# Kernel tuning notes

Measured on AMD Instinct MI355X. Metric: run time of the kernel, lower is better.

Reference implementation:

```python
import jax, jax.numpy as jnp
import numpy as np

N = 500_000   # active voxels
K = 27        # 3x3x3 kernel offsets
CIN = 32
COUT = 64
EPS = 1e-5


def setup_inputs() -> dict:
    key = jax.random.key(0)
    ks = jax.random.split(key, 9)
    x_feats = jax.random.normal(ks[0], (N, CIN), jnp.float32)
    # neighbor map: for each kernel offset k and output voxel i, index of the
    # input voxel contributing through offset k (submanifold conv, stride=1)
    nbr = jax.random.randint(ks[1], (K, N), 0, N, jnp.int32)
    s1 = 1.0 / np.sqrt(K * CIN)
    s2 = 1.0 / np.sqrt(K * COUT)
    w1 = jax.random.normal(ks[2], (K, CIN, COUT), jnp.float32) * s1
    w2 = jax.random.normal(ks[3], (K, COUT, COUT), jnp.float32) * s2
    g1 = jnp.ones((COUT,), jnp.float32)
    b1 = jnp.zeros((COUT,), jnp.float32)
    g2 = jnp.ones((COUT,), jnp.float32)
    b2 = jnp.zeros((COUT,), jnp.float32)
    wid = jax.random.normal(ks[4], (CIN, COUT), jnp.float32) * (1.0 / np.sqrt(CIN))
    gid = jnp.ones((COUT,), jnp.float32)
    bid = jnp.zeros((COUT,), jnp.float32)
    return {"x_feats": x_feats, "nbr": nbr, "w1": w1, "g1": g1, "b1": b1,
            "w2": w2, "g2": g2, "b2": b2, "wid": wid, "gid": gid, "bid": bid}


def _sparse_conv(feats, nbr, W):
    # feats [N, Cin], nbr [K, N], W [K, Cin, Cout]
    # scan over the fixed 27 kernel offsets: gather -> matmul -> accumulate
    def step(acc, kw):
        idx, w = kw
        return acc + feats[idx] @ w, None
    out0 = jnp.zeros((feats.shape[0], W.shape[-1]), feats.dtype)
    out, _ = jax.lax.scan(step, out0, (nbr, W))
    return out


def _bn(x, g, b):
    # training-mode BatchNorm1d over the voxel axis (biased variance, as torch)
    m = jnp.mean(x, axis=0)
    v = jnp.var(x, axis=0)
    return (x - m) * jax.lax.rsqrt(v + EPS) * g + b


def reference(x_feats, nbr, w1, g1, b1, w2, g2, b2, wid, gid, bid):
    h = jax.nn.relu(_bn(_sparse_conv(x_feats, nbr, w1), g1, b1))
    h = _bn(_sparse_conv(h, nbr, w2), g2, b2)
    ident = _bn(x_feats @ wid, gid, bid)
    return jax.nn.relu(h + ident)
```

## Files before the change

### kernel.cpp

```cpp
#include <hip/hip_runtime.h>

#define NV 500000
#define KOFF 27
#define CIN_ 32
#define COUT_ 64
#define EPS_ 1e-5f

typedef __attribute__((ext_vector_type(8))) _Float16 half8;
typedef __attribute__((ext_vector_type(4))) float floatx4;


__global__ void zero_stats_kernel(float* __restrict__ s) {
  if (threadIdx.x < 384) s[threadIdx.x] = 0.f;
}

__global__ __launch_bounds__(256) void cast_x_kernel(
    const float* __restrict__ x, _Float16* __restrict__ xh) {
  size_t q = (size_t)blockIdx.x * 256 + threadIdx.x;
  if (q >= (size_t)NV * CIN_ / 8) return;
  const float4* xp = (const float4*)x;
  float4 a = xp[2 * q], b = xp[2 * q + 1];
  half8 h;
  h[0] = (_Float16)a.x; h[1] = (_Float16)a.y; h[2] = (_Float16)a.z; h[3] = (_Float16)a.w;
  h[4] = (_Float16)b.x; h[5] = (_Float16)b.y; h[6] = (_Float16)b.z; h[7] = (_Float16)b.w;
  ((half8*)xh)[q] = h;
}

__global__ void wtrans_kernel(const float* __restrict__ w,
                              _Float16* __restrict__ wT, int CI) {
  int t = blockIdx.x * 256 + threadIdx.x;
  int total = KOFF * CI * COUT_;
  if (t >= total) return;
  int k = t / (CI * COUT_);
  int r = t % (CI * COUT_);
  int co = r / CI;
  int ci = r % CI;
  wT[t] = (_Float16)w[(k * CI + ci) * COUT_ + co];
}


template<int CI>
__device__ __forceinline__ void stageB(const _Float16* __restrict__ wT,
                                       _Float16* __restrict__ lds,
                                       int k0, int kp, int tid) {
  __syncthreads();
  const int segs = CI / 8;
  const int chunks = kp * COUT_ * segs;
  for (int idx = tid; idx < chunks; idx += 1024) {
    int row = idx / segs;
    int s = idx - row * segs;
    half8 v = *(const half8*)(wT + ((size_t)k0 * COUT_ + row) * CI + s * 8);
    *(half8*)(lds + (size_t)row * (CI + 8) + s * 8) = v;
  }
  __syncthreads();
}

template<int CI, int KPC, int D>
__device__ __forceinline__ void run_phase(
    const half8* __restrict__ fp, const int* __restrict__ nbr,
    const _Float16* __restrict__ lds, int k0,
    int v0, int v1, int m, int quad, floatx4 acc[2][4]) {
  constexpr int SEG = CI / 32;
  constexpr int ROWH8 = CI / 8;

  int j0[KPC], j1[KPC];
#pragma unroll
  for (int k = 0; k < KPC; ++k) {
    j0[k] = nbr[(k0 + k) * NV + v0] * ROWH8;
    j1[k] = nbr[(k0 + k) * NV + v1] * ROWH8;
  }

  half8 ring[D][2][SEG];
#pragma unroll
  for (int p = 0; p < D; ++p) {
#pragma unroll
    for (int s = 0; s < SEG; ++s) {
      ring[p][0][s] = fp[(size_t)j0[p] + s * 4 + quad];
      ring[p][1][s] = fp[(size_t)j1[p] + s * 4 + quad];
    }
  }

#pragma unroll
  for (int k = 0; k < KPC; ++k) {
    const _Float16* bk = lds + (size_t)k * COUT_ * (CI + 8);
#pragma unroll
    for (int s = 0; s < SEG; ++s) {
#pragma unroll
      for (int nf = 0; nf < 4; ++nf) {
        half8 bf = *(const half8*)(bk + (nf * 16 + m) * (CI + 8) + s * 32 + quad * 8);
        acc[0][nf] = __builtin_amdgcn_mfma_f32_16x16x32_f16(ring[k % D][0][s], bf, acc[0][nf], 0, 0, 0);
        acc[1][nf] = __builtin_amdgcn_mfma_f32_16x16x32_f16(ring[k % D][1][s], bf, acc[1][nf], 0, 0, 0);
      }
    }
    if (k + D < KPC) {
#pragma unroll
      for (int s = 0; s < SEG; ++s) {
        ring[k % D][0][s] = fp[(size_t)j0[k + D] + s * 4 + quad];
        ring[k % D][1][s] = fp[(size_t)j1[k + D] + s * 4 + quad];
      }
    }
  }
}

template<int CI, bool WF16>
__global__ __launch_bounds__(1024, 4) void conv_mfma_v3(
    const _Float16* __restrict__ feats, const int* __restrict__ nbr,
    const _Float16* __restrict__ wT, float* __restrict__ outF,
    _Float16* __restrict__ outH) {
  constexpr int LDSH = (CI == 64) ? 7 * 64 * 72 : 9 * 64 * 40;
  __shared__ __align__(16) _Float16 ldsB[LDSH];

  int tid = threadIdx.x;
  int wave = tid >> 6, lane = tid & 63;
  int m = lane & 15, quad = lane >> 4;
  int vbase = (blockIdx.x * 16 + wave) * 32;
  int v0 = vbase + m;
  int v1 = vbase + 16 + m;
  v0 = v0 < NV ? v0 : NV - 1;
  v1 = v1 < NV ? v1 : NV - 1;
  const half8* fp = (const half8*)feats;

  floatx4 acc[2][4];
#pragma unroll
  for (int g = 0; g < 2; ++g)
#pragma unroll
    for (int nf = 0; nf < 4; ++nf) acc[g][nf] = (floatx4){0.f, 0.f, 0.f, 0.f};

  if constexpr (CI == 64) {
    stageB<CI>(wT, ldsB, 0, 7, tid);
    run_phase<CI, 7, 3>(fp, nbr, ldsB, 0, v0, v1, m, quad, acc);
    stageB<CI>(wT, ldsB, 7, 7, tid);
    run_phase<CI, 7, 3>(fp, nbr, ldsB, 7, v0, v1, m, quad, acc);
    stageB<CI>(wT, ldsB, 14, 7, tid);
    run_phase<CI, 7, 3>(fp, nbr, ldsB, 14, v0, v1, m, quad, acc);
    stageB<CI>(wT, ldsB, 21, 6, tid);
    run_phase<CI, 6, 3>(fp, nbr, ldsB, 21, v0, v1, m, quad, acc);
  } else {
    stageB<CI>(wT, ldsB, 0, 9, tid);
    run_phase<CI, 9, 4>(fp, nbr, ldsB, 0, v0, v1, m, quad, acc);
    stageB<CI>(wT, ldsB, 9, 9, tid);
    run_phase<CI, 9, 4>(fp, nbr, ldsB, 9, v0, v1, m, quad, acc);
    stageB<CI>(wT, ldsB, 18, 9, tid);
    run_phase<CI, 9, 4>(fp, nbr, ldsB, 18, v0, v1, m, quad, acc);
  }

#pragma unroll
  for (int g = 0; g < 2; ++g)
#pragma unroll
    for (int nf = 0; nf < 4; ++nf)
#pragma unroll
      for (int r = 0; r < 4; ++r) {
        int row = vbase + g * 16 + quad * 4 + r;
        if (row < NV) {
          size_t o = (size_t)row * COUT_ + nf * 16 + m;
          if (WF16) outH[o] = (_Float16)acc[g][nf][r];
          else outF[o] = acc[g][nf][r];
        }
      }
}


__global__ __launch_bounds__(256) void stats_f16_kernel(
    const _Float16* __restrict__ y, float* __restrict__ sums) {
  int lane = threadIdx.x & 63;
  int r0 = blockIdx.x * 4 + (threadIdx.x >> 6);
  int stride = gridDim.x * 4;
  float s = 0.f, ss = 0.f;
  for (int r = r0; r < NV; r += stride) {
    float v = (float)y[(size_t)r * COUT_ + lane];
    s += v;
    ss = fmaf(v, v, ss);
  }
  __shared__ float ls[128];
  if (threadIdx.x < 128) ls[threadIdx.x] = 0.f;
  __syncthreads();
  atomicAdd(&ls[lane], s);
  atomicAdd(&ls[64 + lane], ss);
  __syncthreads();
  if (threadIdx.x < 128) atomicAdd(&sums[threadIdx.x], ls[threadIdx.x]);
}

__global__ __launch_bounds__(256) void stats_f32_kernel(
    const float* __restrict__ y, float* __restrict__ sums) {
  int lane = threadIdx.x & 63;
  int r0 = blockIdx.x * 4 + (threadIdx.x >> 6);
  int stride = gridDim.x * 4;
  float s = 0.f, ss = 0.f;
  for (int r = r0; r < NV; r += stride) {
    float v = y[(size_t)r * COUT_ + lane];
    s += v;
    ss = fmaf(v, v, ss);
  }
  __shared__ float ls[128];
  if (threadIdx.x < 128) ls[threadIdx.x] = 0.f;
  __syncthreads();
  atomicAdd(&ls[lane], s);
  atomicAdd(&ls[64 + lane], ss);
  __syncthreads();
  if (threadIdx.x < 128) atomicAdd(&sums[threadIdx.x], ls[threadIdx.x]);
}

__global__ __launch_bounds__(256) void ident_stats_kernel(
    const float* __restrict__ x, const float* __restrict__ wid,
    float* __restrict__ sums) {
  int lane = threadIdx.x & 63;
  int wv = blockIdx.x * 4 + (threadIdx.x >> 6);
  int nw = gridDim.x * 4;
  float wcol[CIN_];
#pragma unroll
  for (int ci = 0; ci < CIN_; ++ci) wcol[ci] = wid[ci * COUT_ + lane];
  float s = 0.f, ss = 0.f;
  for (int v = wv; v < NV; v += nw) {
    const float* xr = x + (size_t)v * CIN_;
    float d = 0.f;
#pragma unroll
    for (int ci = 0; ci < CIN_; ++ci) d = fmaf(xr[ci], wcol[ci], d);
    s += d;
    ss = fmaf(d, d, ss);
  }
  __shared__ float ls[128];
  if (threadIdx.x < 128) ls[threadIdx.x] = 0.f;
  __syncthreads();
  atomicAdd(&ls[lane], s);
  atomicAdd(&ls[64 + lane], ss);
  __syncthreads();
  if (threadIdx.x < 128) atomicAdd(&sums[threadIdx.x], ls[threadIdx.x]);
}

__global__ void finalize_kernel(const float* __restrict__ sums,
                                const float* __restrict__ g,
                                const float* __restrict__ b,
                                float* __restrict__ out) {
  int c = threadIdx.x;
  float m = sums[c] * (1.0f / NV);
  float var = sums[64 + c] * (1.0f / NV) - m * m;
  float sc = g[c] / sqrtf(var + EPS_);
  out[c] = sc;
  out[64 + c] = b[c] - m * sc;
}

__global__ __launch_bounds__(256) void bnrelu_f16_kernel(
    _Float16* __restrict__ y, const float* __restrict__ scsh) {
  size_t q = (size_t)blockIdx.x * 256 + threadIdx.x;
  if (q >= (size_t)NV * COUT_ / 8) return;
  int c0 = (int)(q & 7) * 8;
  half8 v = ((const half8*)y)[q];
#pragma unroll
  for (int jj = 0; jj < 8; ++jj) {
    float f = fmaxf(fmaf((float)v[jj], scsh[c0 + jj], scsh[64 + c0 + jj]), 0.f);
    v[jj] = (_Float16)f;
  }
  ((half8*)y)[q] = v;
}

__global__ __launch_bounds__(256) void final_kernel(
    const float* __restrict__ x, const float* __restrict__ wid,
    float* __restrict__ y2out, const float* __restrict__ ss2,
    const float* __restrict__ ssid) {
  int lane = threadIdx.x & 63;
  int wv = blockIdx.x * 4 + (threadIdx.x >> 6);
  int nw = gridDim.x * 4;
  float wcol[CIN_];
#pragma unroll
  for (int ci = 0; ci < CIN_; ++ci) wcol[ci] = wid[ci * COUT_ + lane];
  float sc2 = ss2[lane], sh2 = ss2[64 + lane];
  float sci = ssid[lane], shi = ssid[64 + lane];
  for (int v = wv; v < NV; v += nw) {
    const float* xr = x + (size_t)v * CIN_;
    float d = 0.f;
#pragma unroll
    for (int ci = 0; ci < CIN_; ++ci) d = fmaf(xr[ci], wcol[ci], d);
    size_t o = (size_t)v * COUT_ + lane;
    float r = fmaf(y2out[o], sc2, sh2) + fmaf(d, sci, shi);
    y2out[o] = fmaxf(r, 0.f);
  }
}

extern "C" void kernel_launch(void* const* d_in, const int* in_sizes, int n_in,
                              void* d_out, int out_size, void* d_ws, size_t ws_size,
                              hipStream_t stream) {
  const float* x   = (const float*)d_in[0];
  const int*   nbr = (const int*)d_in[1];
  const float* w1  = (const float*)d_in[2];
  const float* g1  = (const float*)d_in[3];
  const float* b1  = (const float*)d_in[4];
  const float* w2  = (const float*)d_in[5];
  const float* g2  = (const float*)d_in[6];
  const float* b2  = (const float*)d_in[7];
  const float* wid = (const float*)d_in[8];
  const float* gid = (const float*)d_in[9];
  const float* bid = (const float*)d_in[10];
  float* out = (float*)d_out;

  _Float16* y1h = (_Float16*)d_ws;
  _Float16* xh  = y1h + (size_t)NV * COUT_;
  _Float16* wT1 = xh + (size_t)NV * CIN_;
  _Float16* wT2 = wT1 + KOFF * COUT_ * CIN_;
  float*    st  = (float*)(wT2 + KOFF * COUT_ * COUT_);

  const int NWG = (NV + 511) / 512;

  zero_stats_kernel<<<1, 384, 0, stream>>>(st);
  cast_x_kernel<<<(NV * CIN_ / 8 + 255) / 256, 256, 0, stream>>>(x, xh);
  wtrans_kernel<<<(KOFF * CIN_ * COUT_ + 255) / 256, 256, 0, stream>>>(w1, wT1, CIN_);
  wtrans_kernel<<<(KOFF * COUT_ * COUT_ + 255) / 256, 256, 0, stream>>>(w2, wT2, COUT_);

  conv_mfma_v3<CIN_, true><<<NWG, 1024, 0, stream>>>(xh, nbr, wT1, nullptr, y1h);
  stats_f16_kernel<<<2048, 256, 0, stream>>>(y1h, st + 0);
  ident_stats_kernel<<<2048, 256, 0, stream>>>(x, wid, st + 256);
  finalize_kernel<<<1, 64, 0, stream>>>(st + 0, g1, b1, st + 384);
  finalize_kernel<<<1, 64, 0, stream>>>(st + 256, gid, bid, st + 640);
  bnrelu_f16_kernel<<<(NV * COUT_ / 8 + 255) / 256, 256, 0, stream>>>(y1h, st + 384);

  conv_mfma_v3<COUT_, false><<<NWG, 1024, 0, stream>>>(y1h, nbr, wT2, out, nullptr);
  stats_f32_kernel<<<2048, 256, 0, stream>>>(out, st + 128);
  finalize_kernel<<<1, 64, 0, stream>>>(st + 128, g2, b2, st + 512);
  final_kernel<<<4096, 256, 0, stream>>>(x, wid, out, st + 512, st + 640);
}
```

Measured before the change: 1.187 ms.

## Fuse BN statistics into conv epilogues and merge prep kernels

```diff
diff --git a/kernel.cpp b/kernel.cpp
--- a/kernel.cpp
+++ b/kernel.cpp
@@ -14,28 +14,67 @@
   if (threadIdx.x < 384) s[threadIdx.x] = 0.f;
 }
 
-__global__ __launch_bounds__(256) void cast_x_kernel(
-    const float* __restrict__ x, _Float16* __restrict__ xh) {
-  size_t q = (size_t)blockIdx.x * 256 + threadIdx.x;
-  if (q >= (size_t)NV * CIN_ / 8) return;
-  const float4* xp = (const float4*)x;
-  float4 a = xp[2 * q], b = xp[2 * q + 1];
-  half8 h;
-  h[0] = (_Float16)a.x; h[1] = (_Float16)a.y; h[2] = (_Float16)a.z; h[3] = (_Float16)a.w;
-  h[4] = (_Float16)b.x; h[5] = (_Float16)b.y; h[6] = (_Float16)b.z; h[7] = (_Float16)b.w;
-  ((half8*)xh)[q] = h;
-}
-
-__global__ void wtrans_kernel(const float* __restrict__ w,
-                              _Float16* __restrict__ wT, int CI) {
-  int t = blockIdx.x * 256 + threadIdx.x;
-  int total = KOFF * CI * COUT_;
-  if (t >= total) return;
-  int k = t / (CI * COUT_);
-  int r = t % (CI * COUT_);
-  int co = r / CI;
-  int ci = r % CI;
-  wT[t] = (_Float16)w[(k * CI + ci) * COUT_ + co];
+#define CAST_BLKS ((NV * CIN_ / 8 + 255) / 256)
+#define WT1_BLKS ((KOFF * CIN_ * COUT_ + 255) / 256)
+#define WT2_BLKS ((KOFF * COUT_ * COUT_ + 255) / 256)
+#define IDST_BLKS 2048
+
+__global__ __launch_bounds__(256) void prep_kernel(
+    const float* __restrict__ x, _Float16* __restrict__ xh,
+    const float* __restrict__ w1, _Float16* __restrict__ wT1,
+    const float* __restrict__ w2, _Float16* __restrict__ wT2,
+    const float* __restrict__ wid, float* __restrict__ idsums) {
+  int b = blockIdx.x;
+  if (b < CAST_BLKS) {
+    size_t q = (size_t)b * 256 + threadIdx.x;
+    if (q >= (size_t)NV * CIN_ / 8) return;
+    const float4* xp = (const float4*)x;
+    float4 a = xp[2 * q], c = xp[2 * q + 1];
+    half8 h;
+    h[0] = (_Float16)a.x; h[1] = (_Float16)a.y; h[2] = (_Float16)a.z; h[3] = (_Float16)a.w;
+    h[4] = (_Float16)c.x; h[5] = (_Float16)c.y; h[6] = (_Float16)c.z; h[7] = (_Float16)c.w;
+    ((half8*)xh)[q] = h;
+  } else if (b < CAST_BLKS + WT1_BLKS) {
+    int t = (b - CAST_BLKS) * 256 + threadIdx.x;
+    if (t >= KOFF * CIN_ * COUT_) return;
+    int k = t / (CIN_ * COUT_);
+    int r = t % (CIN_ * COUT_);
+    int co = r / CIN_;
+    int ci = r % CIN_;
+    wT1[t] = (_Float16)w1[(k * CIN_ + ci) * COUT_ + co];
+  } else if (b < CAST_BLKS + WT1_BLKS + WT2_BLKS) {
+    int t = (b - CAST_BLKS - WT1_BLKS) * 256 + threadIdx.x;
+    if (t >= KOFF * COUT_ * COUT_) return;
+    int k = t / (COUT_ * COUT_);
+    int r = t % (COUT_ * COUT_);
+    int co = r / COUT_;
+    int ci = r % COUT_;
+    wT2[t] = (_Float16)w2[(k * COUT_ + ci) * COUT_ + co];
+  } else {
+    int bb = b - CAST_BLKS - WT1_BLKS - WT2_BLKS;
+    int lane = threadIdx.x & 63;
+    int wv = bb * 4 + (threadIdx.x >> 6);
+    int nw = IDST_BLKS * 4;
+    float wcol[CIN_];
+#pragma unroll
+    for (int ci = 0; ci < CIN_; ++ci) wcol[ci] = wid[ci * COUT_ + lane];
+    float s = 0.f, ss = 0.f;
+    for (int v = wv; v < NV; v += nw) {
+      const float* xr = x + (size_t)v * CIN_;
+      float d = 0.f;
+#pragma unroll
+      for (int ci = 0; ci < CIN_; ++ci) d = fmaf(xr[ci], wcol[ci], d);
+      s += d;
+      ss = fmaf(d, d, ss);
+    }
+    __shared__ float ls[128];
+    if (threadIdx.x < 128) ls[threadIdx.x] = 0.f;
+    __syncthreads();
+    atomicAdd(&ls[lane], s);
+    atomicAdd(&ls[64 + lane], ss);
+    __syncthreads();
+    if (threadIdx.x < 128) atomicAdd(&idsums[threadIdx.x], ls[threadIdx.x]);
+  }
 }
 
 
@@ -103,12 +142,13 @@
 }
 
 template<int CI, bool WF16>
-__global__ __launch_bounds__(1024, 4) void conv_mfma_v3(
+__global__ __launch_bounds__(1024, 4) void conv_mfma_v9(
     const _Float16* __restrict__ feats, const int* __restrict__ nbr,
     const _Float16* __restrict__ wT, float* __restrict__ outF,
-    _Float16* __restrict__ outH) {
+    _Float16* __restrict__ outH, float* __restrict__ stOut) {
   constexpr int LDSH = (CI == 64) ? 7 * 64 * 72 : 9 * 64 * 40;
   __shared__ __align__(16) _Float16 ldsB[LDSH];
+  __shared__ float bs[128];
 
   int tid = threadIdx.x;
   int wave = tid >> 6, lane = tid & 63;
@@ -119,6 +159,8 @@
   v0 = v0 < NV ? v0 : NV - 1;
   v1 = v1 < NV ? v1 : NV - 1;
   const half8* fp = (const half8*)feats;
+
+  if (tid < 128) bs[tid] = 0.f;
 
   floatx4 acc[2][4];
 #pragma unroll
@@ -144,6 +186,9 @@
     run_phase<CI, 9, 4>(fp, nbr, ldsB, 18, v0, v1, m, quad, acc);
   }
 
+  float s4[4], q4[4];
+#pragma unroll
+  for (int nf = 0; nf < 4; ++nf) { s4[nf] = 0.f; q4[nf] = 0.f; }
 #pragma unroll
   for (int g = 0; g < 2; ++g)
 #pragma unroll
@@ -152,119 +197,77 @@
       for (int r = 0; r < 4; ++r) {
         int row = vbase + g * 16 + quad * 4 + r;
         if (row < NV) {
+          float v = acc[g][nf][r];
           size_t o = (size_t)row * COUT_ + nf * 16 + m;
-          if (WF16) outH[o] = (_Float16)acc[g][nf][r];
-          else outF[o] = acc[g][nf][r];
+          if (WF16) outH[o] = (_Float16)v;
+          else outF[o] = v;
+          s4[nf] += v;
+          q4[nf] = fmaf(v, v, q4[nf]);
         }
       }
-}
-
-
-__global__ __launch_bounds__(256) void stats_f16_kernel(
-    const _Float16* __restrict__ y, float* __restrict__ sums) {
-  int lane = threadIdx.x & 63;
-  int r0 = blockIdx.x * 4 + (threadIdx.x >> 6);
-  int stride = gridDim.x * 4;
-  float s = 0.f, ss = 0.f;
-  for (int r = r0; r < NV; r += stride) {
-    float v = (float)y[(size_t)r * COUT_ + lane];
-    s += v;
-    ss = fmaf(v, v, ss);
-  }
-  __shared__ float ls[128];
-  if (threadIdx.x < 128) ls[threadIdx.x] = 0.f;
+#pragma unroll
+  for (int nf = 0; nf < 4; ++nf) {
+    s4[nf] += __shfl_xor(s4[nf], 16); s4[nf] += __shfl_xor(s4[nf], 32);
+    q4[nf] += __shfl_xor(q4[nf], 16); q4[nf] += __shfl_xor(q4[nf], 32);
+  }
+  if (quad == 0) {
+#pragma unroll
+    for (int nf = 0; nf < 4; ++nf) {
+      atomicAdd(&bs[nf * 16 + m], s4[nf]);
+      atomicAdd(&bs[64 + nf * 16 + m], q4[nf]);
+    }
+  }
   __syncthreads();
-  atomicAdd(&ls[lane], s);
-  atomicAdd(&ls[64 + lane], ss);
+  if (tid < 128) atomicAdd(&stOut[tid], bs[tid]);
+}
+
+
+__global__ __launch_bounds__(256) void bnrelu_f16_kernel(
+    _Float16* __restrict__ y, const float* __restrict__ sums,
+    const float* __restrict__ g, const float* __restrict__ b) {
+  __shared__ float scsh[128];
+  if (threadIdx.x < 64) {
+    int c = threadIdx.x;
+    float mm = sums[c] * (1.0f / NV);
+    float var = sums[64 + c] * (1.0f / NV) - mm * mm;
+    float sc = g[c] / sqrtf(var + EPS_);
+    scsh[c] = sc;
+    scsh[64 + c] = b[c] - mm * sc;
+  }
   __syncthreads();
-  if (threadIdx.x < 128) atomicAdd(&sums[threadIdx.x], ls[threadIdx.x]);
-}
-
-__global__ __launch_bounds__(256) void stats_f32_kernel(
-    const float* __restrict__ y, float* __restrict__ sums) {
-  int lane = threadIdx.x & 63;
-  int r0 = blockIdx.x * 4 + (threadIdx.x >> 6);
-  int stride = gridDim.x * 4;
-  float s = 0.f, ss = 0.f;
-  for (int r = r0; r < NV; r += stride) {
-    float v = y[(size_t)r * COUT_ + lane];
-    s += v;
-    ss = fmaf(v, v, ss);
-  }
-  __shared__ float ls[128];
-  if (threadIdx.x < 128) ls[threadIdx.x] = 0.f;
-  __syncthreads();
-  atomicAdd(&ls[lane], s);
-  atomicAdd(&ls[64 + lane], ss);
-  __syncthreads();
-  if (threadIdx.x < 128) atomicAdd(&sums[threadIdx.x], ls[threadIdx.x]);
-}
-
-__global__ __launch_bounds__(256) void ident_stats_kernel(
+  size_t q = (size_t)blockIdx.x * 256 + threadIdx.x;
+  if (q >= (size_t)NV * COUT_ / 8) return;
+  int c0 = (int)(q & 7) * 8;
+  half8 v = ((const half8*)y)[q];
+#pragma unroll
+  for (int jj = 0; jj < 8; ++jj) {
+    float f = fmaxf(fmaf((float)v[jj], scsh[c0 + jj], scsh[64 + c0 + jj]), 0.f);
+    v[jj] = (_Float16)f;
+  }
+  ((half8*)y)[q] = v;
+}
+
+
+__global__ __launch_bounds__(256) void final_kernel(
     const float* __restrict__ x, const float* __restrict__ wid,
-    float* __restrict__ sums) {
+    float* __restrict__ y2out, const float* __restrict__ sums2,
+    const float* __restrict__ sumsid,
+    const float* __restrict__ g2, const float* __restrict__ b2,
+    const float* __restrict__ gid, const float* __restrict__ bid) {
   int lane = threadIdx.x & 63;
   int wv = blockIdx.x * 4 + (threadIdx.x >> 6);
   int nw = gridDim.x * 4;
   float wcol[CIN_];
 #pragma unroll
   for (int ci = 0; ci < CIN_; ++ci) wcol[ci] = wid[ci * COUT_ + lane];
-  float s = 0.f, ss = 0.f;
-  for (int v = wv; v < NV; v += nw) {
-    const float* xr = x + (size_t)v * CIN_;
-    float d = 0.f;
-#pragma unroll
-    for (int ci = 0; ci < CIN_; ++ci) d = fmaf(xr[ci], wcol[ci], d);
-    s += d;
-    ss = fmaf(d, d, ss);
-  }
-  __shared__ float ls[128];
-  if (threadIdx.x < 128) ls[threadIdx.x] = 0.f;
-  __syncthreads();
-  atomicAdd(&ls[lane], s);
-  atomicAdd(&ls[64 + lane], ss);
-  __syncthreads();
-  if (threadIdx.x < 128) atomicAdd(&sums[threadIdx.x], ls[threadIdx.x]);
-}
-
-__global__ void finalize_kernel(const float* __restrict__ sums,
-                                const float* __restrict__ g,
-                                const float* __restrict__ b,
-                                float* __restrict__ out) {
-  int c = threadIdx.x;
-  float m = sums[c] * (1.0f / NV);
-  float var = sums[64 + c] * (1.0f / NV) - m * m;
-  float sc = g[c] / sqrtf(var + EPS_);
-  out[c] = sc;
-  out[64 + c] = b[c] - m * sc;
-}
-
-__global__ __launch_bounds__(256) void bnrelu_f16_kernel(
-    _Float16* __restrict__ y, const float* __restrict__ scsh) {
-  size_t q = (size_t)blockIdx.x * 256 + threadIdx.x;
-  if (q >= (size_t)NV * COUT_ / 8) return;
-  int c0 = (int)(q & 7) * 8;
-  half8 v = ((const half8*)y)[q];
-#pragma unroll
-  for (int jj = 0; jj < 8; ++jj) {
-    float f = fmaxf(fmaf((float)v[jj], scsh[c0 + jj], scsh[64 + c0 + jj]), 0.f);
-    v[jj] = (_Float16)f;
-  }
-  ((half8*)y)[q] = v;
-}
-
-__global__ __launch_bounds__(256) void final_kernel(
-    const float* __restrict__ x, const float* __restrict__ wid,
-    float* __restrict__ y2out, const float* __restrict__ ss2,
-    const float* __restrict__ ssid) {
-  int lane = threadIdx.x & 63;
-  int wv = blockIdx.x * 4 + (threadIdx.x >> 6);
-  int nw = gridDim.x * 4;
-  float wcol[CIN_];
-#pragma unroll
-  for (int ci = 0; ci < CIN_; ++ci) wcol[ci] = wid[ci * COUT_ + lane];
-  float sc2 = ss2[lane], sh2 = ss2[64 + lane];
-  float sci = ssid[lane], shi = ssid[64 + lane];
+  float m2 = sums2[lane] * (1.0f / NV);
+  float var2 = sums2[64 + lane] * (1.0f / NV) - m2 * m2;
+  float sc2 = g2[lane] / sqrtf(var2 + EPS_);
+  float sh2 = b2[lane] - m2 * sc2;
+  float mi = sumsid[lane] * (1.0f / NV);
+  float vari = sumsid[64 + lane] * (1.0f / NV) - mi * mi;
+  float sci = gid[lane] / sqrtf(vari + EPS_);
+  float shi = bid[lane] - mi * sci;
   for (int v = wv; v < NV; v += nw) {
     const float* xr = x + (size_t)v * CIN_;
     float d = 0.f;
@@ -299,21 +302,15 @@
   float*    st  = (float*)(wT2 + KOFF * COUT_ * COUT_);
 
   const int NWG = (NV + 511) / 512;
+  const int PREP_BLKS = CAST_BLKS + WT1_BLKS + WT2_BLKS + IDST_BLKS;
 
   zero_stats_kernel<<<1, 384, 0, stream>>>(st);
-  cast_x_kernel<<<(NV * CIN_ / 8 + 255) / 256, 256, 0, stream>>>(x, xh);
-  wtrans_kernel<<<(KOFF * CIN_ * COUT_ + 255) / 256, 256, 0, stream>>>(w1, wT1, CIN_);
-  wtrans_kernel<<<(KOFF * COUT_ * COUT_ + 255) / 256, 256, 0, stream>>>(w2, wT2, COUT_);
-
-  conv_mfma_v3<CIN_, true><<<NWG, 1024, 0, stream>>>(xh, nbr, wT1, nullptr, y1h);
-  stats_f16_kernel<<<2048, 256, 0, stream>>>(y1h, st + 0);
-  ident_stats_kernel<<<2048, 256, 0, stream>>>(x, wid, st + 256);
-  finalize_kernel<<<1, 64, 0, stream>>>(st + 0, g1, b1, st + 384);
-  finalize_kernel<<<1, 64, 0, stream>>>(st + 256, gid, bid, st + 640);
-  bnrelu_f16_kernel<<<(NV * COUT_ / 8 + 255) / 256, 256, 0, stream>>>(y1h, st + 384);
-
-  conv_mfma_v3<COUT_, false><<<NWG, 1024, 0, stream>>>(y1h, nbr, wT2, out, nullptr);
-  stats_f32_kernel<<<2048, 256, 0, stream>>>(out, st + 128);
-  finalize_kernel<<<1, 64, 0, stream>>>(st + 128, g2, b2, st + 512);
-  final_kernel<<<4096, 256, 0, stream>>>(x, wid, out, st + 512, st + 640);
-}
+  prep_kernel<<<PREP_BLKS, 256, 0, stream>>>(x, xh, w1, wT1, w2, wT2, wid, st + 256);
+
+  conv_mfma_v9<CIN_, true><<<NWG, 1024, 0, stream>>>(xh, nbr, wT1, nullptr, y1h, st + 0);
+  bnrelu_f16_kernel<<<(NV * COUT_ / 8 + 255) / 256, 256, 0, stream>>>(y1h, st + 0, g1, b1);
+
+  conv_mfma_v9<COUT_, false><<<NWG, 1024, 0, stream>>>(y1h, nbr, wT2, out, nullptr, st + 128);
+  final_kernel<<<4096, 256, 0, stream>>>(x, wid, out, st + 128, st + 256,
+                                         g2, b2, gid, bid);
+}
```

After: 1.059 ms. 10.8% less time.
